# Kernel tuning notes

Measured on AMD Instinct MI355X. Metric: run time of the kernel, lower is better.

## Reference

```python
import jax, jax.numpy as jnp
import numpy as np

H = 768       # hidden_dim
NH = 12       # num_heads
HD = H // NH  # head_dim = 64


def setup_inputs() -> dict:
    key = jax.random.key(0)
    ks = jax.random.split(key, 5)
    scale = 1.0 / np.sqrt(H)
    x = jax.random.normal(ks[0], (16, 1024, H), dtype=jnp.float32)
    W_qkv = jax.random.normal(ks[1], (H, 3 * H), dtype=jnp.float32) * scale
    b_qkv = jnp.zeros((3 * H,), dtype=jnp.float32)
    W_proj = jax.random.normal(ks[2], (H, H), dtype=jnp.float32) * scale
    b_proj = jnp.zeros((H,), dtype=jnp.float32)
    return {"x": x, "W_qkv": W_qkv, "b_qkv": b_qkv, "W_proj": W_proj, "b_proj": b_proj}


def reference(x, W_qkv, b_qkv, W_proj, b_proj):
    bsz, seq_len, hidden = x.shape
    qkv = x @ W_qkv + b_qkv                              # [B,S,3H]
    q, k, v = jnp.split(qkv, 3, axis=-1)
    def heads(t):
        return t.reshape(bsz, seq_len, NH, HD).transpose(0, 2, 1, 3)  # [B,NH,S,HD]
    q, k, v = heads(q), heads(k), heads(v)
    scores = jnp.einsum('bhqd,bhkd->bhqk', q, k) / jnp.sqrt(jnp.float32(HD))
    causal = jnp.tril(jnp.ones((seq_len, seq_len), dtype=bool))
    scores = jnp.where(causal, scores, jnp.finfo(scores.dtype).min)
    attn = jax.nn.softmax(scores, axis=-1)
    out = jnp.einsum('bhqk,bhkd->bhqd', attn, v)         # [B,NH,S,HD]
    out = out.transpose(0, 2, 1, 3).reshape(bsz, seq_len, hidden)
    return out @ W_proj + b_proj
```

## Files before the change

kernel.cpp:

```cpp
#include <hip/hip_runtime.h>

#define H 768
#define NH 12
#define HD 64
#define BSZ 16
#define SEQ 1024
#define MTOK (BSZ * SEQ)
#define N3H (3 * H)

typedef __attribute__((ext_vector_type(8))) short bf16x8;
typedef __attribute__((ext_vector_type(4))) float f32x4;
typedef __attribute__((ext_vector_type(16))) float f32x16;
typedef __attribute__((ext_vector_type(8))) unsigned short us8;
typedef __attribute__((ext_vector_type(4))) unsigned short us4;

__device__ __forceinline__ unsigned short f2bf(float f) {
    union { float f; unsigned u; } v; v.f = f;
    unsigned r = v.u + 0x7fffu + ((v.u >> 16) & 1u);
    return (unsigned short)(r >> 16);
}

typedef __attribute__((address_space(1))) const unsigned int gu32_t;
typedef __attribute__((address_space(3))) unsigned int lu32_t;
__device__ __forceinline__ void glds16(const void* g, void* l) {
    __builtin_amdgcn_global_load_lds((gu32_t*)g, (lu32_t*)l, 16, 0, 0);
}

__global__ __launch_bounds__(256) void cvt_bf16(
    const float* __restrict__ in, unsigned short* __restrict__ out, int n)
{
    int i = (blockIdx.x * 256 + threadIdx.x) * 8;
    if (i >= n) return;
    float4 a = *(const float4*)(in + i);
    float4 b = *(const float4*)(in + i + 4);
    us8 o;
    o[0]=f2bf(a.x); o[1]=f2bf(a.y); o[2]=f2bf(a.z); o[3]=f2bf(a.w);
    o[4]=f2bf(b.x); o[5]=f2bf(b.y); o[6]=f2bf(b.z); o[7]=f2bf(b.w);
    *(us8*)(out + i) = o;
}

__global__ __launch_bounds__(256) void tconv_bf16(
    const float* __restrict__ in, unsigned short* __restrict__ out, int Kd, int Nd)
{
    __shared__ float tile[64][65];
    int t = threadIdx.x;
    int n0 = blockIdx.x * 64, k0 = blockIdx.y * 64;
    #pragma unroll
    for (int r = 0; r < 4; ++r) {
        int kl = r * 16 + (t >> 4);
        float4 v = *(const float4*)(&in[(size_t)(k0 + kl) * Nd + n0 + (t & 15) * 4]);
        tile[kl][(t & 15) * 4 + 0] = v.x; tile[kl][(t & 15) * 4 + 1] = v.y;
        tile[kl][(t & 15) * 4 + 2] = v.z; tile[kl][(t & 15) * 4 + 3] = v.w;
    }
    __syncthreads();
    int nl = t >> 2, kc = (t & 3) * 16;
    us8 o0, o1;
    #pragma unroll
    for (int kk = 0; kk < 8; ++kk) o0[kk] = f2bf(tile[kc + kk][nl]);
    #pragma unroll
    for (int kk = 0; kk < 8; ++kk) o1[kk] = f2bf(tile[kc + 8 + kk][nl]);
    size_t ob = (size_t)(n0 + nl) * Kd + k0 + kc;
    *(us8*)(&out[ob]) = o0;
    *(us8*)(&out[ob + 8]) = o1;
}

__global__ __launch_bounds__(256) void gemm_bf16(
    const unsigned short* __restrict__ A, const unsigned short* __restrict__ BT,
    const float* __restrict__ bias, void* __restrict__ Cout,
    int M, int N, int K, int write_f32, int qscale_end)
{
    __shared__ char lds[65536];
    const char* Ac = (const char*)A;
    const char* Bc = (const char*)BT;
    int t = threadIdx.x;
    int l = t & 63, w = t >> 6;
    int l16 = l & 15, l4 = l >> 4;
    int wm = w >> 1, wn = w & 1;

    int chunk = (int)gridDim.x >> 3;
    int lin = (blockIdx.x & 7) * chunk + (blockIdx.x >> 3);
    int nbx = N >> 7;
    int bx = lin % nbx, by = lin / nbx;
    int rowBase = by * 128, colBase = bx * 128;

    f32x4 acc[4][4];
    #pragma unroll
    for (int i = 0; i < 4; ++i)
        #pragma unroll
        for (int j = 0; j < 4; ++j) acc[i][j] = (f32x4){0, 0, 0, 0};

    auto STAGE = [&](int k0, int bi) {
        char* As = lds + bi * 32768;
        char* Bs = As + 16384;
        #pragma unroll
        for (int i = 0; i < 4; ++i) {
            int c = t + i * 256;
            int row = c >> 3;
            int src = ((c & 7) * 16) ^ ((row & 7) << 4);
            glds16(Ac + ((size_t)(rowBase + row) * K + k0) * 2 + src, As + c * 16);
            glds16(Bc + ((size_t)(colBase + row) * K + k0) * 2 + src, Bs + c * 16);
        }
    };

    STAGE(0, 0);
    int nk = K >> 6;
    for (int kt = 0; kt < nk; ++kt) {
        int bi = kt & 1;
        if (kt + 1 < nk) {
            STAGE((kt + 1) << 6, bi ^ 1);
            asm volatile("s_waitcnt vmcnt(8)" ::: "memory");
        } else {
            asm volatile("s_waitcnt vmcnt(0)" ::: "memory");
        }
        __builtin_amdgcn_s_barrier();

        const char* As = lds + bi * 32768;
        const char* Bs = As + 16384;
        #pragma unroll
        for (int kh = 0; kh < 2; ++kh) {
            bf16x8 af[4], bfr[4];
            #pragma unroll
            for (int mi = 0; mi < 4; ++mi) {
                int row = wm * 64 + mi * 16 + l16;
                af[mi] = *(const bf16x8*)(As + row * 128 + ((l4 * 16 + kh * 64) ^ ((row & 7) << 4)));
            }
            #pragma unroll
            for (int ni = 0; ni < 4; ++ni) {
                int row = wn * 64 + ni * 16 + l16;
                bfr[ni] = *(const bf16x8*)(Bs + row * 128 + ((l4 * 16 + kh * 64) ^ ((row & 7) << 4)));
            }
            #pragma unroll
            for (int mi = 0; mi < 4; ++mi)
                #pragma unroll
                for (int ni = 0; ni < 4; ++ni)
                    acc[mi][ni] = __builtin_amdgcn_mfma_f32_16x16x32_bf16(
                        af[mi], bfr[ni], acc[mi][ni], 0, 0, 0);
        }
        __builtin_amdgcn_s_barrier();
    }

    #pragma unroll
    for (int ni = 0; ni < 4; ++ni) {
        int col = colBase + wn * 64 + ni * 16 + l16;
        float bb = bias ? bias[col] : 0.f;
        float mul = (col < qscale_end) ? 0.125f : 1.0f;
        #pragma unroll
        for (int mi = 0; mi < 4; ++mi) {
            #pragma unroll
            for (int j = 0; j < 4; ++j) {
                int row = rowBase + wm * 64 + mi * 16 + l4 * 4 + j;
                float v = (acc[mi][ni][j] + bb) * mul;
                if (write_f32) ((float*)Cout)[(size_t)row * N + col] = v;
                else ((unsigned short*)Cout)[(size_t)row * N + col] = f2bf(v);
            }
        }
    }
}

__global__ __launch_bounds__(256) void vtrans(
    const unsigned short* __restrict__ qkvb, unsigned short* __restrict__ vt)
{
    __shared__ char tile[64 * 128];
    int t = threadIdx.x;
    int st = blockIdx.x, h = blockIdx.y, b = blockIdx.z;
    int s0 = st * 64;
    {
        int s = t >> 2, dc = (t & 3) * 16;
        size_t g = (size_t)(b * SEQ + s0 + s) * N3H + 2 * H + h * HD + dc;
        us8 v0 = *(const us8*)(&qkvb[g]);
        us8 v1 = *(const us8*)(&qkvb[g + 8]);
        *(us8*)(tile + s * 128 + ((dc * 2) ^ ((s & 7) << 4))) = v0;
        *(us8*)(tile + s * 128 + ((dc * 2 + 16) ^ ((s & 7) << 4))) = v1;
    }
    __syncthreads();
    int d = t >> 2, sc = (t & 3) * 16;
    us8 o0, o1;
    #pragma unroll
    for (int kk = 0; kk < 8; ++kk) {
        int s = sc + kk;
        o0[kk] = *(const unsigned short*)(tile + s * 128 + ((d * 2) ^ ((s & 7) << 4)));
    }
    #pragma unroll
    for (int kk = 0; kk < 8; ++kk) {
        int s = sc + 8 + kk;
        o1[kk] = *(const unsigned short*)(tile + s * 128 + ((d * 2) ^ ((s & 7) << 4)));
    }
    size_t ob = ((size_t)((b * NH + h) * 64 + d)) * SEQ + s0 + sc;
    *(us8*)(&vt[ob]) = o0;
    *(us8*)(&vt[ob + 8]) = o1;
}

__global__ __launch_bounds__(256, 4) void attn_mfma(
    const unsigned short* __restrict__ qkvb,
    const unsigned short* __restrict__ vt,
    unsigned short* __restrict__ aout)
{
    __shared__ char lds[32768];
    char* Kbuf = lds;
    char* Vbuf = lds + 16384;
    int t = threadIdx.x;
    int l = t & 63, w = t >> 6;
    int l31 = l & 31, b5 = l >> 5;

    int lin = ((blockIdx.x & 7) * 192) + (blockIdx.x >> 3);
    int qb = 7 - (lin & 7);
    int bh = lin >> 3;
    int h = bh % NH, b = bh / NH;

    int wq = qb * 128 + w * 32;
    int sw31 = (l31 & 7) << 4;
    int nt = 2 * qb + 2;
    int bhh = b * NH + h;
    const char* qkvc = (const char*)qkvb;
    const char* vtc  = (const char*)vt;

    bf16x8 qB[4];
    {
        const unsigned short* qrow =
            qkvb + (size_t)(b * SEQ + wq + l31) * N3H + h * HD + b5 * 8;
        #pragma unroll
        for (int m = 0; m < 4; ++m) qB[m] = *(const bf16x8*)(qrow + m * 16);
    }

    auto STAGE = [&](int kt, int bi) {
        #pragma unroll
        for (int i = 0; i < 2; ++i) {
            int c = t + i * 256;
            int row = c >> 3;
            int src = ((c & 7) * 16) ^ ((row & 7) << 4);
            glds16(qkvc + ((size_t)(b * SEQ + kt * 64 + row) * N3H + H + h * HD) * 2 + src,
                   Kbuf + bi * 8192 + c * 16);
        }
        #pragma unroll
        for (int i = 0; i < 2; ++i) {
            int c = t + i * 256;
            int row = c >> 3;
            int src = ((c & 7) * 16) ^ ((row & 7) << 4);
            glds16(vtc + (((size_t)(bhh * 64 + row)) * SEQ + kt * 64) * 2 + src,
                   Vbuf + bi * 8192 + c * 16);
        }
    };

    STAGE(0, 0);
    __syncthreads();

    f32x16 o0, o1;
    #pragma unroll
    for (int r = 0; r < 16; ++r) { o0[r] = 0.f; o1[r] = 0.f; }
    float mrun = -1e30f, lrun = 0.f;

    for (int kt = 0; kt < nt; ++kt) {
        int bi = kt & 1;
        if (kt + 1 < nt) {
            STAGE(kt + 1, bi ^ 1);
            asm volatile("s_waitcnt vmcnt(4)" ::: "memory");
        } else {
            asm volatile("s_waitcnt vmcnt(0)" ::: "memory");
        }
        __builtin_amdgcn_s_barrier();

        int ktbase = kt * 64;
        if (ktbase <= wq + 31) {
            const char* Kb = Kbuf + bi * 8192;
            const char* Vb = Vbuf + bi * 8192;

            f32x16 s[2];
            __builtin_amdgcn_s_setprio(1);
            #pragma unroll
            for (int st2 = 0; st2 < 2; ++st2) {
                f32x16 acc;
                #pragma unroll
                for (int r = 0; r < 16; ++r) acc[r] = 0.f;
                #pragma unroll
                for (int m = 0; m < 4; ++m) {
                    int row = st2 * 32 + l31;
                    bf16x8 kf = *(const bf16x8*)(Kb + row * 128 + ((m * 32 + b5 * 16) ^ sw31));
                    acc = __builtin_amdgcn_mfma_f32_32x32x16_bf16(kf, qB[m], acc, 0, 0, 0);
                }
                s[st2] = acc;
            }
            __builtin_amdgcn_s_setprio(0);

            if (ktbase + 63 > wq) {
                int q = wq + l31;
                #pragma unroll
                for (int st2 = 0; st2 < 2; ++st2)
                    #pragma unroll
                    for (int r = 0; r < 16; ++r) {
                        int key = ktbase + st2 * 32 + (r & 3) + 8 * (r >> 2) + 4 * b5;
                        if (key > q) s[st2][r] = -3e38f;
                    }
            }

            float mx = s[0][0];
            #pragma unroll
            for (int r = 1; r < 16; ++r) mx = fmaxf(mx, s[0][r]);
            #pragma unroll
            for (int r = 0; r < 16; ++r) mx = fmaxf(mx, s[1][r]);
            mx = fmaxf(mx, __shfl_xor(mx, 32, 64));
            if (!__all(mx - mrun <= 8.f)) {
                float mnew = fmaxf(mrun, mx);
                float sc = __expf(mrun - mnew);
                mrun = mnew;
                lrun *= sc;
                #pragma unroll
                for (int r = 0; r < 16; ++r) { o0[r] *= sc; o1[r] *= sc; }
            }
            float rs = 0.f;
            #pragma unroll
            for (int st2 = 0; st2 < 2; ++st2)
                #pragma unroll
                for (int r = 0; r < 16; ++r) {
                    float p = __expf(s[st2][r] - mrun);
                    s[st2][r] = p;
                    rs += p;
                }
            rs += __shfl_xor(rs, 32, 64);
            lrun += rs;

            bf16x8 pB[4];
            #pragma unroll
            for (int wd = 0; wd < 4; ++wd) {
                int st2 = wd >> 1, hf = (wd & 1) * 8;
                unsigned pk0 = (unsigned)f2bf(s[st2][hf + 0]) | ((unsigned)f2bf(s[st2][hf + 1]) << 16);
                unsigned pk1 = (unsigned)f2bf(s[st2][hf + 2]) | ((unsigned)f2bf(s[st2][hf + 3]) << 16);
                unsigned pk2 = (unsigned)f2bf(s[st2][hf + 4]) | ((unsigned)f2bf(s[st2][hf + 5]) << 16);
                unsigned pk3 = (unsigned)f2bf(s[st2][hf + 6]) | ((unsigned)f2bf(s[st2][hf + 7]) << 16);
                unsigned snd0 = b5 ? pk0 : pk2;
                unsigned snd1 = b5 ? pk1 : pk3;
                unsigned r0 = (unsigned)__shfl_xor((int)snd0, 32, 64);
                unsigned r1 = (unsigned)__shfl_xor((int)snd1, 32, 64);
                union { unsigned u[4]; bf16x8 v; } cvt;
                cvt.u[0] = b5 ? r0 : pk0;
                cvt.u[1] = b5 ? r1 : pk1;
                cvt.u[2] = b5 ? pk2 : r0;
                cvt.u[3] = b5 ? pk3 : r1;
                pB[wd] = cvt.v;
            }

            __builtin_amdgcn_s_setprio(1);
            #pragma unroll
            for (int wd = 0; wd < 4; ++wd) {
                bf16x8 v0 = *(const bf16x8*)(Vb + l31 * 128 + ((wd * 32 + b5 * 16) ^ sw31));
                o0 = __builtin_amdgcn_mfma_f32_32x32x16_bf16(v0, pB[wd], o0, 0, 0, 0);
                bf16x8 v1 = *(const bf16x8*)(Vb + (32 + l31) * 128 + ((wd * 32 + b5 * 16) ^ sw31));
                o1 = __builtin_amdgcn_mfma_f32_32x32x16_bf16(v1, pB[wd], o1, 0, 0, 0);
            }
            __builtin_amdgcn_s_setprio(0);
        }
        __builtin_amdgcn_s_barrier();
    }

    float inv = 1.f / lrun;
    size_t tok = (size_t)(b * SEQ + wq + l31);
    #pragma unroll
    for (int g = 0; g < 4; ++g) {
        us4 w0, w1;
        #pragma unroll
        for (int j = 0; j < 4; ++j) {
            w0[j] = f2bf(o0[g * 4 + j] * inv);
            w1[j] = f2bf(o1[g * 4 + j] * inv);
        }
        int d0 = g * 8 + b5 * 4;
        *(us4*)(&aout[tok * H + h * HD + d0]) = w0;
        *(us4*)(&aout[tok * H + h * HD + 32 + d0]) = w1;
    }
}

extern "C" void kernel_launch(void* const* d_in, const int* in_sizes, int n_in,
                              void* d_out, int out_size, void* d_ws, size_t ws_size,
                              hipStream_t stream) {
    const float* x      = (const float*)d_in[0];
    const float* W_qkv  = (const float*)d_in[1];
    const float* b_qkv  = (const float*)d_in[2];
    const float* W_proj = (const float*)d_in[3];
    const float* b_proj = (const float*)d_in[4];
    float* outp = (float*)d_out;

    char* ws = (char*)d_ws;
    unsigned short* xbf    = (unsigned short*)ws;  ws += (size_t)MTOK * H * 2;
    unsigned short* wqkvT  = (unsigned short*)ws;  ws += (size_t)N3H * H * 2;
    unsigned short* wprojT = (unsigned short*)ws;  ws += (size_t)H * H * 2;
    unsigned short* qkvb   = (unsigned short*)ws;  ws += (size_t)MTOK * N3H * 2;
    unsigned short* vtb    = (unsigned short*)ws;  ws += (size_t)BSZ * NH * 64 * SEQ * 2;
    unsigned short* aob    = (unsigned short*)ws;

    cvt_bf16<<<(MTOK * H) / (256 * 8), 256, 0, stream>>>(x, xbf, MTOK * H);
    tconv_bf16<<<dim3(N3H / 64, H / 64), 256, 0, stream>>>(W_qkv, wqkvT, H, N3H);
    tconv_bf16<<<dim3(H / 64, H / 64), 256, 0, stream>>>(W_proj, wprojT, H, H);

    gemm_bf16<<<(N3H / 128) * (MTOK / 128), 256, 0, stream>>>(
        xbf, wqkvT, b_qkv, qkvb, MTOK, N3H, H, 0, H);

    vtrans<<<dim3(SEQ / 64, NH, BSZ), 256, 0, stream>>>(qkvb, vtb);

    attn_mfma<<<(SEQ / 128) * NH * BSZ, 256, 0, stream>>>(qkvb, vtb, aob);

    gemm_bf16<<<(H / 128) * (MTOK / 128), 256, 0, stream>>>(
        aob, wprojT, b_proj, (void*)outp, MTOK, H, H, 1, 0);
}
```

Measured before the change: 311.1 us.

## Merge prep kernels, retile GEMM to 256x128 with 32x32 MFMA, skip masked attention half-tiles

Three conversion kernels become one prep launch that dispatches on block index. The GEMM moves to 256x128 tiles with 32x32x16 MFMA, where each wave owns 64 rows and all 128 columns. In exchange it drops the double-buffered LDS pipeline, so every k-step waits on its own loads with vmcnt(0). The attention kernel skips the second 32-key subtile's QK, softmax and PV work when that subtile lies entirely above the causal diagonal, which removes wasted MFMAs on diagonal tiles.

```diff
diff --git a/kernel.cpp b/kernel.cpp
--- a/kernel.cpp
+++ b/kernel.cpp
@@ -26,25 +26,36 @@
     __builtin_amdgcn_global_load_lds((gu32_t*)g, (lu32_t*)l, 16, 0, 0);
 }
 
-__global__ __launch_bounds__(256) void cvt_bf16(
-    const float* __restrict__ in, unsigned short* __restrict__ out, int n)
-{
-    int i = (blockIdx.x * 256 + threadIdx.x) * 8;
-    if (i >= n) return;
-    float4 a = *(const float4*)(in + i);
-    float4 b = *(const float4*)(in + i + 4);
-    us8 o;
-    o[0]=f2bf(a.x); o[1]=f2bf(a.y); o[2]=f2bf(a.z); o[3]=f2bf(a.w);
-    o[4]=f2bf(b.x); o[5]=f2bf(b.y); o[6]=f2bf(b.z); o[7]=f2bf(b.w);
-    *(us8*)(out + i) = o;
-}
-
-__global__ __launch_bounds__(256) void tconv_bf16(
-    const float* __restrict__ in, unsigned short* __restrict__ out, int Kd, int Nd)
+__global__ __launch_bounds__(256) void prep(
+    const float* __restrict__ x,
+    const float* __restrict__ Wqkv, const float* __restrict__ Wproj,
+    unsigned short* __restrict__ xbf,
+    unsigned short* __restrict__ wqkvT, unsigned short* __restrict__ wprojT)
 {
     __shared__ float tile[64][65];
-    int t = threadIdx.x;
-    int n0 = blockIdx.x * 64, k0 = blockIdx.y * 64;
+    int bx = blockIdx.x, t = threadIdx.x;
+
+    if (bx < 6144) {
+        int i = bx * 2048 + t * 8;
+        float4 a = *(const float4*)(x + i);
+        float4 b = *(const float4*)(x + i + 4);
+        us8 o;
+        o[0]=f2bf(a.x); o[1]=f2bf(a.y); o[2]=f2bf(a.z); o[3]=f2bf(a.w);
+        o[4]=f2bf(b.x); o[5]=f2bf(b.y); o[6]=f2bf(b.z); o[7]=f2bf(b.w);
+        *(us8*)(xbf + i) = o;
+        return;
+    }
+
+    const float* in; unsigned short* out; int Kd, Nd, n0, k0;
+    if (bx < 6576) {
+        int lb = bx - 6144;
+        in = Wqkv; out = wqkvT; Kd = H; Nd = N3H;
+        n0 = (lb % 36) * 64; k0 = (lb / 36) * 64;
+    } else {
+        int lb = bx - 6576;
+        in = Wproj; out = wprojT; Kd = H; Nd = H;
+        n0 = (lb % 12) * 64; k0 = (lb / 12) * 64;
+    }
     #pragma unroll
     for (int r = 0; r < 4; ++r) {
         int kl = r * 16 + (t >> 4);
@@ -69,71 +80,65 @@
     const float* __restrict__ bias, void* __restrict__ Cout,
     int M, int N, int K, int write_f32, int qscale_end)
 {
-    __shared__ char lds[65536];
+    __shared__ char lds[49152];
+    char* As = lds;
+    char* Bs = lds + 32768;
     const char* Ac = (const char*)A;
     const char* Bc = (const char*)BT;
     int t = threadIdx.x;
     int l = t & 63, w = t >> 6;
-    int l16 = l & 15, l4 = l >> 4;
-    int wm = w >> 1, wn = w & 1;
+    int l31 = l & 31, b5 = l >> 5;
 
     int chunk = (int)gridDim.x >> 3;
     int lin = (blockIdx.x & 7) * chunk + (blockIdx.x >> 3);
     int nbx = N >> 7;
     int bx = lin % nbx, by = lin / nbx;
-    int rowBase = by * 128, colBase = bx * 128;
-
-    f32x4 acc[4][4];
-    #pragma unroll
-    for (int i = 0; i < 4; ++i)
-        #pragma unroll
-        for (int j = 0; j < 4; ++j) acc[i][j] = (f32x4){0, 0, 0, 0};
-
-    auto STAGE = [&](int k0, int bi) {
-        char* As = lds + bi * 32768;
-        char* Bs = As + 16384;
+    int rowBase = by * 256, colBase = bx * 128;
+
+    f32x16 acc[2][4];
+    #pragma unroll
+    for (int mi = 0; mi < 2; ++mi)
+        #pragma unroll
+        for (int ni = 0; ni < 4; ++ni)
+            #pragma unroll
+            for (int r = 0; r < 16; ++r) acc[mi][ni][r] = 0.f;
+
+    for (int k0 = 0; k0 < K; k0 += 64) {
+        #pragma unroll
+        for (int i = 0; i < 8; ++i) {
+            int c = t + i * 256;
+            int row = c >> 3;
+            int src = ((c & 7) * 16) ^ ((row & 7) << 4);
+            glds16(Ac + ((size_t)(rowBase + row) * K + k0) * 2 + src, As + c * 16);
+        }
         #pragma unroll
         for (int i = 0; i < 4; ++i) {
             int c = t + i * 256;
             int row = c >> 3;
             int src = ((c & 7) * 16) ^ ((row & 7) << 4);
-            glds16(Ac + ((size_t)(rowBase + row) * K + k0) * 2 + src, As + c * 16);
             glds16(Bc + ((size_t)(colBase + row) * K + k0) * 2 + src, Bs + c * 16);
         }
-    };
-
-    STAGE(0, 0);
-    int nk = K >> 6;
-    for (int kt = 0; kt < nk; ++kt) {
-        int bi = kt & 1;
-        if (kt + 1 < nk) {
-            STAGE((kt + 1) << 6, bi ^ 1);
-            asm volatile("s_waitcnt vmcnt(8)" ::: "memory");
-        } else {
-            asm volatile("s_waitcnt vmcnt(0)" ::: "memory");
-        }
+        asm volatile("s_waitcnt vmcnt(0)" ::: "memory");
         __builtin_amdgcn_s_barrier();
 
-        const char* As = lds + bi * 32768;
-        const char* Bs = As + 16384;
-        #pragma unroll
-        for (int kh = 0; kh < 2; ++kh) {
-            bf16x8 af[4], bfr[4];
-            #pragma unroll
-            for (int mi = 0; mi < 4; ++mi) {
-                int row = wm * 64 + mi * 16 + l16;
-                af[mi] = *(const bf16x8*)(As + row * 128 + ((l4 * 16 + kh * 64) ^ ((row & 7) << 4)));
+        #pragma unroll
+        for (int ks = 0; ks < 4; ++ks) {
+            bf16x8 af[2], bfr[4];
+            #pragma unroll
+            for (int mi = 0; mi < 2; ++mi) {
+                int row = w * 64 + mi * 32 + l31;
+                af[mi] = *(const bf16x8*)(As + row * 128 + ((ks * 32 + b5 * 16) ^ ((row & 7) << 4)));
             }
             #pragma unroll
             for (int ni = 0; ni < 4; ++ni) {
-                int row = wn * 64 + ni * 16 + l16;
-                bfr[ni] = *(const bf16x8*)(Bs + row * 128 + ((l4 * 16 + kh * 64) ^ ((row & 7) << 4)));
-            }
-            #pragma unroll
-            for (int mi = 0; mi < 4; ++mi)
+                int row = ni * 32 + l31;
+                bfr[ni] = *(const bf16x8*)(Bs + row * 128 + ((ks * 32 + b5 * 16) ^ ((row & 7) << 4)));
+            }
+            #pragma unroll
+            for (int mi = 0; mi < 2; ++mi)
                 #pragma unroll
                 for (int ni = 0; ni < 4; ++ni)
-                    acc[mi][ni] = __builtin_amdgcn_mfma_f32_16x16x32_bf16(
+                    acc[mi][ni] = __builtin_amdgcn_mfma_f32_32x32x16_bf16(
                         af[mi], bfr[ni], acc[mi][ni], 0, 0, 0);
         }
         __builtin_amdgcn_s_barrier();
@@ -141,15 +146,15 @@
 
     #pragma unroll
     for (int ni = 0; ni < 4; ++ni) {
-        int col = colBase + wn * 64 + ni * 16 + l16;
+        int col = colBase + ni * 32 + l31;
         float bb = bias ? bias[col] : 0.f;
         float mul = (col < qscale_end) ? 0.125f : 1.0f;
         #pragma unroll
-        for (int mi = 0; mi < 4; ++mi) {
-            #pragma unroll
-            for (int j = 0; j < 4; ++j) {
-                int row = rowBase + wm * 64 + mi * 16 + l4 * 4 + j;
-                float v = (acc[mi][ni][j] + bb) * mul;
+        for (int mi = 0; mi < 2; ++mi) {
+            #pragma unroll
+            for (int reg = 0; reg < 16; ++reg) {
+                int row = rowBase + w * 64 + mi * 32 + (reg & 3) + 8 * (reg >> 2) + 4 * b5;
+                float v = (acc[mi][ni][reg] + bb) * mul;
                 if (write_f32) ((float*)Cout)[(size_t)row * N + col] = v;
                 else ((unsigned short*)Cout)[(size_t)row * N + col] = f2bf(v);
             }
@@ -263,40 +268,64 @@
         if (ktbase <= wq + 31) {
             const char* Kb = Kbuf + bi * 8192;
             const char* Vb = Vbuf + bi * 8192;
-
-            f32x16 s[2];
+            bool two = (ktbase + 32 <= wq + 31);
+
+            f32x16 s0, s1;
             __builtin_amdgcn_s_setprio(1);
-            #pragma unroll
-            for (int st2 = 0; st2 < 2; ++st2) {
-                f32x16 acc;
-                #pragma unroll
-                for (int r = 0; r < 16; ++r) acc[r] = 0.f;
+            {
+                f32x16 a;
+                #pragma unroll
+                for (int r = 0; r < 16; ++r) a[r] = 0.f;
                 #pragma unroll
                 for (int m = 0; m < 4; ++m) {
-                    int row = st2 * 32 + l31;
-                    bf16x8 kf = *(const bf16x8*)(Kb + row * 128 + ((m * 32 + b5 * 16) ^ sw31));
-                    acc = __builtin_amdgcn_mfma_f32_32x32x16_bf16(kf, qB[m], acc, 0, 0, 0);
+                    bf16x8 kf = *(const bf16x8*)(Kb + l31 * 128 + ((m * 32 + b5 * 16) ^ sw31));
+                    a = __builtin_amdgcn_mfma_f32_32x32x16_bf16(kf, qB[m], a, 0, 0, 0);
                 }
-                s[st2] = acc;
+                s0 = a;
+            }
+            if (two) {
+                f32x16 a;
+                #pragma unroll
+                for (int r = 0; r < 16; ++r) a[r] = 0.f;
+                #pragma unroll
+                for (int m = 0; m < 4; ++m) {
+                    bf16x8 kf = *(const bf16x8*)(Kb + (32 + l31) * 128 + ((m * 32 + b5 * 16) ^ sw31));
+                    a = __builtin_amdgcn_mfma_f32_32x32x16_bf16(kf, qB[m], a, 0, 0, 0);
+                }
+                s1 = a;
             }
             __builtin_amdgcn_s_setprio(0);
 
-            if (ktbase + 63 > wq) {
-                int q = wq + l31;
-                #pragma unroll
-                for (int st2 = 0; st2 < 2; ++st2)
-                    #pragma unroll
-                    for (int r = 0; r < 16; ++r) {
-                        int key = ktbase + st2 * 32 + (r & 3) + 8 * (r >> 2) + 4 * b5;
-                        if (key > q) s[st2][r] = -3e38f;
-                    }
-            }
-
-            float mx = s[0][0];
-            #pragma unroll
-            for (int r = 1; r < 16; ++r) mx = fmaxf(mx, s[0][r]);
-            #pragma unroll
-            for (int r = 0; r < 16; ++r) mx = fmaxf(mx, s[1][r]);
+            int q = wq + l31;
+            if (ktbase + 31 > wq) {
+                #pragma unroll
+                for (int r = 0; r < 16; ++r) {
+                    int key = ktbase + (r & 3) + 8 * (r >> 2) + 4 * b5;
+                    if (key > q) s0[r] = -3e38f;
+                }
+            }
+            if (two && (ktbase + 63 > wq)) {
+                #pragma unroll
+                for (int r = 0; r < 16; ++r) {
+                    int key = ktbase + 32 + (r & 3) + 8 * (r >> 2) + 4 * b5;
+                    if (key > q) s1[r] = -3e38f;
+                }
+            }
+
+            float m01 = fmaxf(s0[0], s0[1]), m23 = fmaxf(s0[2], s0[3]);
+            float m45 = fmaxf(s0[4], s0[5]), m67 = fmaxf(s0[6], s0[7]);
+            float m89 = fmaxf(s0[8], s0[9]), mab = fmaxf(s0[10], s0[11]);
+            float mcd = fmaxf(s0[12], s0[13]), mef = fmaxf(s0[14], s0[15]);
+            float mx = fmaxf(fmaxf(fmaxf(m01, m23), fmaxf(m45, m67)),
+                             fmaxf(fmaxf(m89, mab), fmaxf(mcd, mef)));
+            if (two) {
+                float n01 = fmaxf(s1[0], s1[1]), n23 = fmaxf(s1[2], s1[3]);
+                float n45 = fmaxf(s1[4], s1[5]), n67 = fmaxf(s1[6], s1[7]);
+                float n89 = fmaxf(s1[8], s1[9]), nab = fmaxf(s1[10], s1[11]);
+                float ncd = fmaxf(s1[12], s1[13]), nef = fmaxf(s1[14], s1[15]);
+                mx = fmaxf(mx, fmaxf(fmaxf(fmaxf(n01, n23), fmaxf(n45, n67)),
+                                     fmaxf(fmaxf(n89, nab), fmaxf(ncd, nef))));
+            }
             mx = fmaxf(mx, __shfl_xor(mx, 32, 64));
             if (!__all(mx - mrun <= 8.f)) {
                 float mnew = fmaxf(mrun, mx);
@@ -308,24 +337,32 @@
             }
             float rs = 0.f;
             #pragma unroll
-            for (int st2 = 0; st2 < 2; ++st2)
+            for (int r = 0; r < 16; ++r) {
+                float p = __expf(s0[r] - mrun);
+                s0[r] = p;
+                rs += p;
+            }
+            if (two) {
                 #pragma unroll
                 for (int r = 0; r < 16; ++r) {
-                    float p = __expf(s[st2][r] - mrun);
-                    s[st2][r] = p;
+                    float p = __expf(s1[r] - mrun);
+                    s1[r] = p;
                     rs += p;
                 }
+            }
             rs += __shfl_xor(rs, 32, 64);
             lrun += rs;
 
             bf16x8 pB[4];
             #pragma unroll
             for (int wd = 0; wd < 4; ++wd) {
-                int st2 = wd >> 1, hf = (wd & 1) * 8;
-                unsigned pk0 = (unsigned)f2bf(s[st2][hf + 0]) | ((unsigned)f2bf(s[st2][hf + 1]) << 16);
-                unsigned pk1 = (unsigned)f2bf(s[st2][hf + 2]) | ((unsigned)f2bf(s[st2][hf + 3]) << 16);
-                unsigned pk2 = (unsigned)f2bf(s[st2][hf + 4]) | ((unsigned)f2bf(s[st2][hf + 5]) << 16);
-                unsigned pk3 = (unsigned)f2bf(s[st2][hf + 6]) | ((unsigned)f2bf(s[st2][hf + 7]) << 16);
+                if (wd >= 2 && !two) break;
+                const f32x16& sv = (wd < 2) ? s0 : s1;
+                int hf = (wd & 1) * 8;
+                unsigned pk0 = (unsigned)f2bf(sv[hf + 0]) | ((unsigned)f2bf(sv[hf + 1]) << 16);
+                unsigned pk1 = (unsigned)f2bf(sv[hf + 2]) | ((unsigned)f2bf(sv[hf + 3]) << 16);
+                unsigned pk2 = (unsigned)f2bf(sv[hf + 4]) | ((unsigned)f2bf(sv[hf + 5]) << 16);
+                unsigned pk3 = (unsigned)f2bf(sv[hf + 6]) | ((unsigned)f2bf(sv[hf + 7]) << 16);
                 unsigned snd0 = b5 ? pk0 : pk2;
                 unsigned snd1 = b5 ? pk1 : pk3;
                 unsigned r0 = (unsigned)__shfl_xor((int)snd0, 32, 64);
@@ -341,6 +378,7 @@
             __builtin_amdgcn_s_setprio(1);
             #pragma unroll
             for (int wd = 0; wd < 4; ++wd) {
+                if (wd >= 2 && !two) break;
                 bf16x8 v0 = *(const bf16x8*)(Vb + l31 * 128 + ((wd * 32 + b5 * 16) ^ sw31));
                 o0 = __builtin_amdgcn_mfma_f32_32x32x16_bf16(v0, pB[wd], o0, 0, 0, 0);
                 bf16x8 v1 = *(const bf16x8*)(Vb + (32 + l31) * 128 + ((wd * 32 + b5 * 16) ^ sw31));
@@ -385,17 +423,15 @@
     unsigned short* vtb    = (unsigned short*)ws;  ws += (size_t)BSZ * NH * 64 * SEQ * 2;
     unsigned short* aob    = (unsigned short*)ws;
 
-    cvt_bf16<<<(MTOK * H) / (256 * 8), 256, 0, stream>>>(x, xbf, MTOK * H);
-    tconv_bf16<<<dim3(N3H / 64, H / 64), 256, 0, stream>>>(W_qkv, wqkvT, H, N3H);
-    tconv_bf16<<<dim3(H / 64, H / 64), 256, 0, stream>>>(W_proj, wprojT, H, H);
-
-    gemm_bf16<<<(N3H / 128) * (MTOK / 128), 256, 0, stream>>>(
+    prep<<<6720, 256, 0, stream>>>(x, W_qkv, W_proj, xbf, wqkvT, wprojT);
+
+    gemm_bf16<<<(MTOK / 256) * (N3H / 128), 256, 0, stream>>>(
         xbf, wqkvT, b_qkv, qkvb, MTOK, N3H, H, 0, H);
 
     vtrans<<<dim3(SEQ / 64, NH, BSZ), 256, 0, stream>>>(qkvb, vtb);
 
     attn_mfma<<<(SEQ / 128) * NH * BSZ, 256, 0, stream>>>(qkvb, vtb, aob);
 
-    gemm_bf16<<<(H / 128) * (MTOK / 128), 256, 0, stream>>>(
+    gemm_bf16<<<(MTOK / 256) * (H / 128), 256, 0, stream>>>(
         aob, wprojT, b_proj, (void*)outp, MTOK, H, H, 1, 0);
 }
```

After: 379.5 us. +22.0%, slower.
